# Kernel tuning notes

Hardware: AMD Instinct MI355X
Metric: run time of the kernel (lower is better)

## Reference

```python
import jax, jax.numpy as jnp
import numpy as np

B, S, D, NH, NKV, HD, FF = 2, 2048, 2048, 16, 8, 128, 8192
EPS = 1e-6
ROPE_THETA = 10000.0


def rmsnorm(x, w):
    return x * jax.lax.rsqrt(jnp.mean(x * x, axis=-1, keepdims=True) + EPS) * w


def rotate_half(x):
    h = x.shape[-1] // 2
    return jnp.concatenate([-x[..., h:], x[..., :h]], axis=-1)


def setup_inputs() -> dict:
    key = jax.random.key(0)
    ks = jax.random.split(key, 32)
    sc = 0.02
    inp = {}
    inp['x'] = jax.random.normal(ks[0], (B, S, D), dtype=jnp.float32)
    pos = jnp.arange(S, dtype=jnp.float32)
    inv = 1.0 / (ROPE_THETA ** (jnp.arange(0, HD, 2, dtype=jnp.float32) / HD))
    fr = jnp.outer(pos, inv)
    emb = jnp.concatenate([fr, fr], axis=-1)  # [S, HD]
    inp['cos'] = jnp.broadcast_to(jnp.cos(emb)[None], (B, S, HD)).astype(jnp.float32)
    inp['sin'] = jnp.broadcast_to(jnp.sin(emb)[None], (B, S, HD)).astype(jnp.float32)
    inp['vision_token_mask'] = jax.random.randint(ks[1], (B, S), 0, 2) > 0
    inp['attn_norm_w'] = jnp.ones((D,), jnp.float32)
    inp['ffn_norm_w'] = jnp.ones((D,), jnp.float32)
    shapes = {
        'wq': (D, NH * HD), 'wk': (D, NKV * HD), 'wv': (D, NKV * HD), 'wo': (NH * HD, D),
        'mm_wq': (D, NH * HD), 'mm_wk': (D, NKV * HD), 'mm_wv': (D, NKV * HD), 'mm_wo': (NH * HD, D),
        'gate_w': (D, FF), 'up_w': (D, FF), 'down_w': (FF, D),
        'mm_gate_w': (D, FF), 'mm_up_w': (D, FF), 'mm_down_w': (FF, D),
    }
    for i, (name, shp) in enumerate(shapes.items()):
        inp[name] = jax.random.normal(ks[2 + i], shp, dtype=jnp.float32) * sc
    for name in ['q_norm_w', 'k_norm_w', 'mm_q_norm_w', 'mm_k_norm_w']:
        inp[name] = jnp.ones((HD,), jnp.float32)
    return inp


def gpt_block(x, cos, sin, mask, attn_norm_w, ffn_norm_w,
              wq, wk, wv, wo, mm_wq, mm_wk, mm_wv, mm_wo,
              q_norm_w, k_norm_w, mm_q_norm_w, mm_k_norm_w,
              gate_w, up_w, down_w, mm_gate_w, mm_up_w, mm_down_w):
    m2 = mask[..., None]            # [B,S,1]
    m4 = mask[:, :, None, None]     # [B,S,1,1]
    h = rmsnorm(x, attn_norm_w)
    # dual-path QKV: text tokens use plain weights, vision tokens use mm_* weights
    q_t = rmsnorm((h @ wq).reshape(B, S, NH, HD), q_norm_w)
    q_v = rmsnorm((h @ mm_wq).reshape(B, S, NH, HD), mm_q_norm_w)
    q = jnp.where(m4, q_v, q_t)
    k_t = rmsnorm((h @ wk).reshape(B, S, NKV, HD), k_norm_w)
    k_v = rmsnorm((h @ mm_wk).reshape(B, S, NKV, HD), mm_k_norm_w)
    k = jnp.where(m4, k_v, k_t)
    v = jnp.where(m2, h @ mm_wv, h @ wv).reshape(B, S, NKV, HD)
    # RoPE (unsqueeze over head dim)
    cu = cos[:, :, None, :]
    su = sin[:, :, None, :]
    q = q * cu + rotate_half(q) * su
    k = k * cu + rotate_half(k) * su
    # GQA repeat + causal attention
    rep = NH // NKV
    k_r = jnp.repeat(k, rep, axis=2)
    v_r = jnp.repeat(v, rep, axis=2)
    scale = 1.0 / jnp.sqrt(jnp.float32(HD))
    scores = jnp.einsum('bqhd,bkhd->bhqk', q, k_r) * scale
    causal = jnp.tril(jnp.ones((S, S), bool))
    scores = jnp.where(causal, scores, jnp.float32(-1e30))
    p = jax.nn.softmax(scores, axis=-1)
    attn = jnp.einsum('bhqk,bkhd->bqhd', p, v_r).reshape(B, S, NH * HD)
    attn_out = jnp.where(m2, attn @ mm_wo, attn @ wo)
    h2 = x + attn_out
    # dual-path SwiGLU FFN
    g = rmsnorm(h2, ffn_norm_w)
    ff_t = (jax.nn.silu(g @ gate_w) * (g @ up_w)) @ down_w
    ff_v = (jax.nn.silu(g @ mm_gate_w) * (g @ mm_up_w)) @ mm_down_w
    return h2 + jnp.where(m2, ff_v, ff_t)


def reference(x, cos, sin, vision_token_mask, attn_norm_w, ffn_norm_w,
              wq, wk, wv, wo, mm_wq, mm_wk, mm_wv, mm_wo,
              q_norm_w, k_norm_w, mm_q_norm_w, mm_k_norm_w,
              gate_w, up_w, down_w, mm_gate_w, mm_up_w, mm_down_w):
    return gpt_block(x, cos, sin, vision_token_mask, attn_norm_w, ffn_norm_w,
                     wq, wk, wv, wo, mm_wq, mm_wk, mm_wv, mm_wo,
                     q_norm_w, k_norm_w, mm_q_norm_w, mm_k_norm_w,
                     gate_w, up_w, down_w, mm_gate_w, mm_up_w, mm_down_w)
```

## Files before the change

kernel.cpp:

```cpp
#include <hip/hip_runtime.h>

typedef unsigned short u16;
typedef __bf16 bf16x8 __attribute__((ext_vector_type(8)));
typedef float f32x4 __attribute__((ext_vector_type(4)));

__device__ __forceinline__ u16 f2bf(float f) {
    unsigned u = __builtin_bit_cast(unsigned, f);
    u += 0x7fffu + ((u >> 16) & 1u);
    return (u16)(u >> 16);
}
__device__ __forceinline__ float bf2f(u16 v) {
    unsigned u = ((unsigned)v) << 16;
    return __builtin_bit_cast(float, u);
}
__device__ __forceinline__ void glds16(const void* g, void* l) {
    __builtin_amdgcn_global_load_lds(
        (const __attribute__((address_space(1))) unsigned*)g,
        (__attribute__((address_space(3))) unsigned*)l, 16, 0, 0);
}

__global__ __launch_bounds__(1024) void build_perm(
    const int* __restrict__ mask, int* __restrict__ perm, int* __restrict__ counts)
{
    __shared__ int sc[1024];
    int t = threadIdx.x;
    int m[4], cnt = 0;
#pragma unroll
    for (int j = 0; j < 4; j++) {
        m[j] = mask[t * 4 + j] != 0;
        cnt += (m[j] == 0);
    }
    sc[t] = cnt;
    __syncthreads();
    for (int off = 1; off < 1024; off <<= 1) {
        int v = (t >= off) ? sc[t - off] : 0;
        __syncthreads();
        sc[t] += v;
        __syncthreads();
    }
    int totT = sc[1023];
    int exT = sc[t] - cnt;
    int exV = t * 4 - exT;
    int pT = exT, pV = totT + exV;
#pragma unroll
    for (int j = 0; j < 4; j++) {
        if (m[j] == 0) perm[pT++] = t * 4 + j;
        else           perm[pV++] = t * 4 + j;
    }
    if (t == 0) { counts[0] = totT; counts[1] = 4096 - totT; }
}

__global__ __launch_bounds__(256) void transpose_bf16(
    const float* __restrict__ W, u16* __restrict__ Wt, int Kd, int Nd)
{
    __shared__ float tile[32][33];
    int k0 = blockIdx.x * 32, n0 = blockIdx.y * 32;
    int tx = threadIdx.x, ty = threadIdx.y;
#pragma unroll
    for (int i = 0; i < 32; i += 8)
        tile[ty + i][tx] = W[(long)(k0 + ty + i) * Nd + n0 + tx];
    __syncthreads();
#pragma unroll
    for (int i = 0; i < 32; i += 8)
        Wt[(long)(n0 + ty + i) * Kd + k0 + tx] = f2bf(tile[tx][ty + i]);
}

__global__ __launch_bounds__(256) void rms_x(
    const float* __restrict__ x, const float* __restrict__ w, u16* __restrict__ out)
{
    long row = blockIdx.x;
    int t = threadIdx.x, wave = t >> 6, lane = t & 63;
    const float4* x4 = (const float4*)(x + row * 2048);
    float4 a = x4[2 * t], b = x4[2 * t + 1];
    float ss = a.x*a.x + a.y*a.y + a.z*a.z + a.w*a.w
             + b.x*b.x + b.y*b.y + b.z*b.z + b.w*b.w;
#pragma unroll
    for (int m = 1; m < 64; m <<= 1) ss += __shfl_xor(ss, m);
    __shared__ float red[4];
    if (lane == 0) red[wave] = ss;
    __syncthreads();
    float tot = red[0] + red[1] + red[2] + red[3];
    float inv = rsqrtf(tot * (1.0f / 2048.0f) + 1e-6f);
    const float4* w4 = (const float4*)w;
    float4 wa = w4[2 * t], wb = w4[2 * t + 1];
    u16* op = out + row * 2048 + t * 8;
    op[0] = f2bf(a.x * inv * wa.x); op[1] = f2bf(a.y * inv * wa.y);
    op[2] = f2bf(a.z * inv * wa.z); op[3] = f2bf(a.w * inv * wa.w);
    op[4] = f2bf(b.x * inv * wb.x); op[5] = f2bf(b.y * inv * wb.y);
    op[6] = f2bf(b.z * inv * wb.z); op[7] = f2bf(b.w * inv * wb.w);
}

template <int EPI, bool PG, bool PC>
__global__ __launch_bounds__(512, 2) void gemmk(
    const u16* __restrict__ A, const u16* __restrict__ Bt0, const u16* __restrict__ Bt1,
    void* __restrict__ Cv, const float* __restrict__ resid,
    const int* __restrict__ perm, const int* __restrict__ counts, int N, int K)
{
    extern __shared__ u16 lds[];
    const int nTn = N >> 8;
    const int nloc = nTn >> 3;
    const int xcd = blockIdx.x & 7, l = blockIdx.x >> 3;
    const int tn = xcd * nloc + (l % nloc);
    const int tm = l / nloc;
    const int nT = counts[0];
    const int tT = (nT + 127) >> 7, tV = (4096 - nT + 127) >> 7;
    if (tm >= tT + tV) return;
    const bool vis = tm >= tT;
    const u16* Bt = vis ? Bt1 : Bt0;
    const int rowbase = vis ? nT + (tm - tT) * 128 : tm * 128;
    const int rowlim = vis ? 4096 : nT;
    const int tid = threadIdx.x;
    const int wave = tid >> 6, lane = tid & 63;
    const int wrbase = (wave >> 2) * 64, wcbase = (wave & 3) * 64;
    const int lr = lane & 15, lg = lane >> 4;
    const int n0 = tn * 256;
    const int t8 = tid >> 3, sp = tid & 7;
    const char* aSrc[2];
    const char* bSrc[4];
#pragma unroll
    for (int c = 0; c < 2; c++) {
        int r = c * 64 + t8;
        int gr = rowbase + r; gr = gr < 4095 ? gr : 4095;
        long ar = PG ? perm[gr] : gr;
        aSrc[c] = (const char*)A + ar * (long)K * 2 + ((sp ^ (r & 7)) << 4);
    }
#pragma unroll
    for (int c = 0; c < 4; c++) {
        int r = c * 64 + t8;
        bSrc[c] = (const char*)Bt + (long)(n0 + r) * K * 2 + ((sp ^ (r & 7)) << 4);
    }
    auto stage = [&](int kt, int bu) {
        char* ab = (char*)lds + bu * 49152;
        char* bb = ab + 16384;
        long ko = (long)kt * 128;
#pragma unroll
        for (int c = 0; c < 2; c++)
            glds16(aSrc[c] + ko, ab + c * 8192 + tid * 16);
#pragma unroll
        for (int c = 0; c < 4; c++)
            glds16(bSrc[c] + ko, bb + c * 8192 + tid * 16);
    };
    auto ldA = [&](int bu, int mi, int kk) -> bf16x8 {
        const char* ab = (const char*)lds + bu * 49152;
        int row = wrbase + mi * 16 + lr;
        int sl = kk * 4 + lg;
        return *(const bf16x8*)(ab + row * 128 + ((sl ^ (row & 7)) << 4));
    };
    auto ldB = [&](int bu, int ni, int kk) -> bf16x8 {
        const char* bb = (const char*)lds + bu * 49152 + 16384;
        int row = wcbase + ni * 16 + lr;
        int sl = kk * 4 + lg;
        return *(const bf16x8*)(bb + row * 128 + ((sl ^ (row & 7)) << 4));
    };

    f32x4 acc[4][4] = {};
    const int nkt = K >> 6;
    stage(0, 0);
    stage(1, 1);
    for (int kt = 0; kt < nkt; ++kt) {
        const int bu = kt % 3;
        if (kt == nkt - 1) asm volatile("s_waitcnt vmcnt(0)" ::: "memory");
        else               asm volatile("s_waitcnt vmcnt(6)" ::: "memory");
        __builtin_amdgcn_s_barrier();
        if (kt + 2 < nkt) stage(kt + 2, (kt + 2) % 3);
#pragma unroll
        for (int kk = 0; kk < 2; kk++) {
            bf16x8 af[4], bq[4];
#pragma unroll
            for (int i = 0; i < 4; i++) af[i] = ldA(bu, i, kk);
#pragma unroll
            for (int j = 0; j < 4; j++) bq[j] = ldB(bu, j, kk);
            __builtin_amdgcn_s_setprio(1);
#pragma unroll
            for (int i = 0; i < 4; i++)
#pragma unroll
                for (int j = 0; j < 4; j++)
                    acc[i][j] = __builtin_amdgcn_mfma_f32_16x16x32_bf16(
                        af[i], bq[j], acc[i][j], 0, 0, 0);
            __builtin_amdgcn_s_setprio(0);
        }
    }
#pragma unroll
    for (int mi = 0; mi < 4; mi++)
#pragma unroll
        for (int r = 0; r < 4; r++) {
            int gr = rowbase + wrbase + mi * 16 + lg * 4 + r;
            if (gr >= rowlim) continue;
            long crow = PC ? (long)perm[gr] : (long)gr;
#pragma unroll
            for (int ni = 0; ni < 4; ni++) {
                long col = n0 + wcbase + ni * 16 + lr;
                long idx = crow * (long)N + col;
                float v = acc[mi][ni][r];
                if (EPI == 1)      ((u16*)Cv)[idx] = f2bf(v);
                else if (EPI == 2) ((float*)Cv)[idx] = resid[idx] + v;
                else if (EPI == 3) {
                    float g = bf2f(((u16*)Cv)[idx]);
                    ((u16*)Cv)[idx] = f2bf(g / (1.0f + __expf(-g)) * v);
                }
            }
        }
}

__global__ __launch_bounds__(256) void qk_fuse(
    const u16* __restrict__ p, const int* __restrict__ mask,
    const float* __restrict__ cs, const float* __restrict__ sn,
    const float* __restrict__ nwt, const float* __restrict__ nwv,
    u16* __restrict__ out, int H, int stride)
{
    int wave = threadIdx.x >> 6, lane = threadIdx.x & 63;
    int gw = blockIdx.x * 4 + wave;
    int tok = gw / H, h = gw % H;
    int b = tok >> 11, s = tok & 2047;
    const u16* src = p + (long)tok * stride + h * 128;
    const float* w = mask[tok] ? nwv : nwt;
    int d = lane * 2;
    float yx = bf2f(src[d]), yy = bf2f(src[d + 1]);
    float ss = yx * yx + yy * yy;
#pragma unroll
    for (int m = 1; m < 64; m <<= 1) ss += __shfl_xor(ss, m);
    float inv = rsqrtf(ss * (1.0f / 128.0f) + 1e-6f);
    float y0 = yx * inv * w[d], y1 = yy * inv * w[d + 1];
    float o0 = __shfl_xor(y0, 32), o1 = __shfl_xor(y1, 32);
    float sgn = (lane < 32) ? -1.0f : 1.0f;
    const float* cp = cs + (long)tok * 128 + d;
    const float* sp = sn + (long)tok * 128 + d;
    float r0 = y0 * cp[0] + sgn * o0 * sp[0];
    float r1 = y1 * cp[1] + sgn * o1 * sp[1];
    u16* op = out + (((long)b * H + h) * 2048 + s) * 128 + d;
    op[0] = f2bf(r0); op[1] = f2bf(r1);
}

__global__ __launch_bounds__(256) void v_fuse(
    const u16* __restrict__ vsrc, u16* __restrict__ outv)
{
    __shared__ u16 tile[32][33];
    int s0 = blockIdx.x * 32, d0 = blockIdx.y * 32;
    int bkv = blockIdx.z, b = bkv >> 3, kv = bkv & 7;
    int tx = threadIdx.x, ty = threadIdx.y;
#pragma unroll
    for (int i = 0; i < 32; i += 8) {
        long tok = (long)b * 2048 + s0 + ty + i;
        tile[ty + i][tx] = vsrc[tok * 2048 + kv * 128 + d0 + tx];
    }
    __syncthreads();
#pragma unroll
    for (int i = 0; i < 32; i += 8)
        outv[(((long)b * 8 + kv) * 128 + d0 + ty + i) * 2048 + s0 + tx] =
            tile[tx][ty + i];
}

__global__ __launch_bounds__(256) void attn_fwd(
    const u16* __restrict__ q, const u16* __restrict__ k,
    const u16* __restrict__ v, u16* __restrict__ out)
{
    __shared__ u16 Ks[32 * 128];
    __shared__ u16 Vs[128 * 32];
    __shared__ u16 Ps[4][16][40];
    const int tid = threadIdx.x, wave = tid >> 6, lane = tid & 63;
    const int lr = lane & 15, lg = lane >> 4;
    const int b = blockIdx.z, h = blockIdx.y, q0 = blockIdx.x * 64;
    const int kvh = h >> 1;
    const u16* qp = q + (((long)b * 16 + h) * 2048 + q0 + wave * 16) * 128;
    bf16x8 qf[4];
#pragma unroll
    for (int f = 0; f < 4; f++)
        qf[f] = *(const bf16x8*)(qp + (long)lr * 128 + f * 32 + lg * 8);
    const char* kbase = (const char*)(k + ((long)b * 8 + kvh) * 2048 * 128);
    const char* vbase = (const char*)(v + ((long)b * 8 + kvh) * 128 * 2048);
    f32x4 o[8] = {};
    float lsum[4] = {};
    const float sc2 = 0.08838834764831845f * 1.44269504088896f;
    const float MB = 16.5f;
    const int ntiles = (q0 + 64) >> 5;
    for (int t = 0; t < ntiles; ++t) {
        int kv0 = t * 32;
        __syncthreads();
#pragma unroll
        for (int j = 0; j < 2; j++) {
            int L = (j * 4 + wave) * 1024 + lane * 16;
            {
                int row = L >> 8, cb = L & 255;
                glds16(kbase + (long)(kv0 + row) * 256 + (cb ^ ((row & 7) << 4)),
                       (char*)Ks + (j * 4 + wave) * 1024);
            }
            {
                int row = L >> 6, cb = L & 63;
                glds16(vbase + (long)row * 4096 + kv0 * 2 + (cb ^ ((row & 3) << 4)),
                       (char*)Vs + (j * 4 + wave) * 1024);
            }
        }
        __syncthreads();
        f32x4 s[2] = {};
#pragma unroll
        for (int sub = 0; sub < 2; ++sub)
#pragma unroll
            for (int f = 0; f < 4; ++f) {
                int row = sub * 16 + lr;
                int cb = (f * 64 + lg * 16) ^ ((row & 7) << 4);
                bf16x8 kf = *(const bf16x8*)((const char*)Ks + row * 256 + cb);
                s[sub] = __builtin_amdgcn_mfma_f32_16x16x32_bf16(qf[f], kf, s[sub], 0, 0, 0);
            }
#pragma unroll
        for (int r = 0; r < 4; r++) {
            int rowg = q0 + wave * 16 + lg * 4 + r;
            float s0 = s[0][r] * sc2 - MB; if (kv0 + lr > rowg)      s0 = -1e30f;
            float s1 = s[1][r] * sc2 - MB; if (kv0 + 16 + lr > rowg) s1 = -1e30f;
            float p0 = exp2f(s0), p1 = exp2f(s1);
            lsum[r] += p0 + p1;
            int prow = lg * 4 + r;
            Ps[wave][prow][lr] = f2bf(p0);
            Ps[wave][prow][16 + lr] = f2bf(p1);
        }
        bf16x8 pf = *(const bf16x8*)&Ps[wave][lr][lg * 8];
#pragma unroll
        for (int ni = 0; ni < 8; ni++) {
            int row = ni * 16 + lr;
            int cb = (lg * 16) ^ ((row & 3) << 4);
            bf16x8 vf = *(const bf16x8*)((const char*)Vs + row * 64 + cb);
            o[ni] = __builtin_amdgcn_mfma_f32_16x16x32_bf16(pf, vf, o[ni], 0, 0, 0);
        }
    }
#pragma unroll
    for (int r = 0; r < 4; r++)
#pragma unroll
        for (int mm = 1; mm < 16; mm <<= 1) lsum[r] += __shfl_xor(lsum[r], mm);
#pragma unroll
    for (int ni = 0; ni < 8; ni++)
#pragma unroll
        for (int r = 0; r < 4; r++) {
            long row = (long)b * 2048 + q0 + wave * 16 + lg * 4 + r;
            out[row * 2048 + h * 128 + ni * 16 + lr] = f2bf(o[ni][r] / lsum[r]);
        }
}

extern "C" void kernel_launch(void* const* d_in, const int* in_sizes, int n_in,
                              void* d_out, int out_size, void* d_ws, size_t ws_size,
                              hipStream_t stream)
{
    const float* x    = (const float*)d_in[0];
    const float* cosp = (const float*)d_in[1];
    const float* sinp = (const float*)d_in[2];
    const int*   mask = (const int*)d_in[3];
    const float* anw  = (const float*)d_in[4];
    const float* fnw  = (const float*)d_in[5];
    const float* wq   = (const float*)d_in[6];
    const float* wk   = (const float*)d_in[7];
    const float* wv   = (const float*)d_in[8];
    const float* wo   = (const float*)d_in[9];
    const float* mwq  = (const float*)d_in[10];
    const float* mwk  = (const float*)d_in[11];
    const float* mwv  = (const float*)d_in[12];
    const float* mwo  = (const float*)d_in[13];
    const float* gw   = (const float*)d_in[14];
    const float* uw   = (const float*)d_in[15];
    const float* dw   = (const float*)d_in[16];
    const float* mgw  = (const float*)d_in[17];
    const float* muw  = (const float*)d_in[18];
    const float* mdw  = (const float*)d_in[19];
    const float* qnw  = (const float*)d_in[20];
    const float* knw  = (const float*)d_in[21];
    const float* mqnw = (const float*)d_in[22];
    const float* mknw = (const float*)d_in[23];

    char* base = (char*)d_ws;
    u16* wT0   = (u16*)(base);
    u16* wT1   = (u16*)(base + (32u << 20));
    u16* hbf   = (u16*)(base + (64u << 20));
    u16* qb    = (u16*)(base + (64u << 20));
    u16* qq    = (u16*)(base + (80u << 20));
    u16* kvb   = (u16*)(base + (96u << 20));
    u16* kb    = (u16*)(base + (112u << 20));
    u16* vb    = (u16*)(base + (120u << 20));
    u16* attnb = (u16*)(base + (128u << 20));
    u16* e1    = (u16*)(base + (80u << 20));
    float* h2  = (float*)(base + (144u << 20));
    u16* gbf   = (u16*)(base + (176u << 20));
    int* perm  = (int*)(base + (192u << 20));
    int* cnts  = perm + 4096;

    hipFuncSetAttribute((const void*)&gemmk<1, true, true>,
                        hipFuncAttributeMaxDynamicSharedMemorySize, 147456);
    hipFuncSetAttribute((const void*)&gemmk<2, true, true>,
                        hipFuncAttributeMaxDynamicSharedMemorySize, 147456);
    hipFuncSetAttribute((const void*)&gemmk<1, true, false>,
                        hipFuncAttributeMaxDynamicSharedMemorySize, 147456);
    hipFuncSetAttribute((const void*)&gemmk<3, true, false>,
                        hipFuncAttributeMaxDynamicSharedMemorySize, 147456);
    hipFuncSetAttribute((const void*)&gemmk<2, false, true>,
                        hipFuncAttributeMaxDynamicSharedMemorySize, 147456);

    dim3 tb(32, 8);
    auto TR = [&](const float* w, u16* dst, int K, int N) {
        transpose_bf16<<<dim3(K / 32, N / 32), tb, 0, stream>>>(w, dst, K, N);
    };

    build_perm<<<1, 1024, 0, stream>>>(mask, perm, cnts);
    rms_x<<<4096, 256, 0, stream>>>(x, anw, hbf);

    TR(wq, wT0, 2048, 2048); TR(mwq, wT1, 2048, 2048);
    gemmk<1, true, true><<<264, 512, 147456, stream>>>(
        hbf, wT0, wT1, (void*)qq, nullptr, perm, cnts, 2048, 2048);
    TR(wk, wT0, 2048, 1024); TR(wv, wT0 + 1024 * 2048, 2048, 1024);
    TR(mwk, wT1, 2048, 1024); TR(mwv, wT1 + 1024 * 2048, 2048, 1024);
    gemmk<1, true, true><<<264, 512, 147456, stream>>>(
        hbf, wT0, wT1, (void*)kvb, nullptr, perm, cnts, 2048, 2048);

    qk_fuse<<<16384, 256, 0, stream>>>(qq, mask, cosp, sinp, qnw, mqnw, qb, 16, 2048);
    qk_fuse<<<8192, 256, 0, stream>>>(kvb, mask, cosp, sinp, knw, mknw, kb, 8, 2048);
    v_fuse<<<dim3(64, 4, 16), tb, 0, stream>>>(kvb + 1024, vb);

    attn_fwd<<<dim3(32, 16, 2), 256, 0, stream>>>(qb, kb, vb, attnb);

    TR(wo, wT0, 2048, 2048); TR(mwo, wT1, 2048, 2048);
    gemmk<2, true, true><<<264, 512, 147456, stream>>>(
        attnb, wT0, wT1, (void*)h2, x, perm, cnts, 2048, 2048);

    rms_x<<<4096, 256, 0, stream>>>(h2, fnw, gbf);

    TR(gw, wT0, 2048, 8192); TR(mgw, wT1, 2048, 8192);
    gemmk<1, true, false><<<1056, 512, 147456, stream>>>(
        gbf, wT0, wT1, (void*)e1, nullptr, perm, cnts, 8192, 2048);
    TR(uw, wT0, 2048, 8192); TR(muw, wT1, 2048, 8192);
    gemmk<3, true, false><<<1056, 512, 147456, stream>>>(
        gbf, wT0, wT1, (void*)e1, nullptr, perm, cnts, 8192, 2048);
    TR(dw, wT0, 8192, 2048); TR(mdw, wT1, 8192, 2048);
    gemmk<2, false, true><<<264, 512, 147456, stream>>>(
        e1, wT0, wT1, (void*)d_out, h2, perm, cnts, 2048, 8192);
}
```

Baseline: 1.225 ms.

## Fuse gate/up GEMMs with SwiGLU epilogue, merge QKV GEMM, remap XCD tiles

Merges the Q and KV projections into one GEMM over a concatenated 4096-wide weight, so the normalized activations are read once and there is one launch fewer. Replaces the separate gate GEMM and the up GEMM with a read-modify-write epilogue by a single gemm_gu kernel. It computes both accumulators on a 128-wide N tile and applies SiLU*up in registers, which removes the bf16 round trip of the gate output. Adds an xcd_map that groups M tiles in chunks of eight per XCD for better L2 reuse. The workspace layout is enlarged to hold two weight buffers at once, and the hardcoded TM=33 assumes 4096 tokens.

```diff
diff --git a/kernel.cpp b/kernel.cpp
--- a/kernel.cpp
+++ b/kernel.cpp
@@ -17,6 +17,21 @@
     __builtin_amdgcn_global_load_lds(
         (const __attribute__((address_space(1))) unsigned*)g,
         (__attribute__((address_space(3))) unsigned*)l, 16, 0, 0);
+}
+
+__device__ __forceinline__ void xcd_map(int bid, int nloc, int& tm, int& tn)
+{
+    const int TM = 33;
+    const int xcd = bid & 7;
+    int l = bid >> 3;
+    const int per = nloc << 3;
+    const int fullC = TM >> 3;
+    const int lFull = fullC * per;
+    int c, tn_l, tmIn;
+    if (l < lFull) { c = l / per; int r = l - c * per; tn_l = r >> 3; tmIn = r & 7; }
+    else { int r = l - lFull; int sc = TM - (fullC << 3); c = fullC; tn_l = r / sc; tmIn = r % sc; }
+    tm = (c << 3) + tmIn;
+    tn = xcd * nloc + tn_l;
 }
 
 __global__ __launch_bounds__(1024) void build_perm(
@@ -97,11 +112,8 @@
     const int* __restrict__ perm, const int* __restrict__ counts, int N, int K)
 {
     extern __shared__ u16 lds[];
-    const int nTn = N >> 8;
-    const int nloc = nTn >> 3;
-    const int xcd = blockIdx.x & 7, l = blockIdx.x >> 3;
-    const int tn = xcd * nloc + (l % nloc);
-    const int tm = l / nloc;
+    int tm, tn;
+    xcd_map(blockIdx.x, N >> 11, tm, tn);
     const int nT = counts[0];
     const int tT = (nT + 127) >> 7, tV = (4096 - nT + 127) >> 7;
     if (tm >= tT + tV) return;
@@ -194,10 +206,104 @@
                 float v = acc[mi][ni][r];
                 if (EPI == 1)      ((u16*)Cv)[idx] = f2bf(v);
                 else if (EPI == 2) ((float*)Cv)[idx] = resid[idx] + v;
-                else if (EPI == 3) {
-                    float g = bf2f(((u16*)Cv)[idx]);
-                    ((u16*)Cv)[idx] = f2bf(g / (1.0f + __expf(-g)) * v);
+            }
+        }
+}
+
+__global__ __launch_bounds__(512, 2) void gemm_gu(
+    const u16* __restrict__ A,
+    const u16* __restrict__ Bg0, const u16* __restrict__ Bg1,
+    const u16* __restrict__ Bu0, const u16* __restrict__ Bu1,
+    u16* __restrict__ C,
+    const int* __restrict__ perm, const int* __restrict__ counts, int N, int K)
+{
+    extern __shared__ u16 lds[];
+    int tm, tn;
+    xcd_map(blockIdx.x, N >> 10, tm, tn);
+    const int nT = counts[0];
+    const int tT = (nT + 127) >> 7, tV = (4096 - nT + 127) >> 7;
+    if (tm >= tT + tV) return;
+    const bool vis = tm >= tT;
+    const u16* Bg = vis ? Bg1 : Bg0;
+    const u16* Bu = vis ? Bu1 : Bu0;
+    const int rowbase = vis ? nT + (tm - tT) * 128 : tm * 128;
+    const int rowlim = vis ? 4096 : nT;
+    const int tid = threadIdx.x;
+    const int wave = tid >> 6, lane = tid & 63;
+    const int wrbase = (wave >> 2) * 64, wcbase = (wave & 3) * 32;
+    const int lr = lane & 15, lg = lane >> 4;
+    const int n0 = tn * 128;
+    const int t8 = tid >> 3, sp = tid & 7;
+    const char *aSrc[2], *gSrc[2], *uSrc[2];
+#pragma unroll
+    for (int c = 0; c < 2; c++) {
+        int r = c * 64 + t8;
+        int gr = rowbase + r; gr = gr < 4095 ? gr : 4095;
+        long ar = (long)perm[gr];
+        aSrc[c] = (const char*)A + ar * (long)K * 2 + ((sp ^ (r & 7)) << 4);
+        gSrc[c] = (const char*)Bg + (long)(n0 + r) * K * 2 + ((sp ^ (r & 7)) << 4);
+        uSrc[c] = (const char*)Bu + (long)(n0 + r) * K * 2 + ((sp ^ (r & 7)) << 4);
+    }
+    auto stage = [&](int kt, int bu) {
+        char* ab = (char*)lds + bu * 49152;
+        long ko = (long)kt * 128;
+#pragma unroll
+        for (int c = 0; c < 2; c++) {
+            glds16(aSrc[c] + ko, ab + c * 8192 + tid * 16);
+            glds16(gSrc[c] + ko, ab + 16384 + c * 8192 + tid * 16);
+            glds16(uSrc[c] + ko, ab + 32768 + c * 8192 + tid * 16);
+        }
+    };
+    auto ld = [&](int bu, int sub, int row, int kk) -> bf16x8 {
+        const char* p = (const char*)lds + bu * 49152 + sub * 16384;
+        int sl = kk * 4 + lg;
+        return *(const bf16x8*)(p + row * 128 + ((sl ^ (row & 7)) << 4));
+    };
+
+    f32x4 accg[4][2] = {}, accu[4][2] = {};
+    const int nkt = K >> 6;
+    stage(0, 0);
+    stage(1, 1);
+    for (int kt = 0; kt < nkt; ++kt) {
+        const int bu = kt % 3;
+        if (kt == nkt - 1) asm volatile("s_waitcnt vmcnt(0)" ::: "memory");
+        else               asm volatile("s_waitcnt vmcnt(6)" ::: "memory");
+        __builtin_amdgcn_s_barrier();
+        if (kt + 2 < nkt) stage(kt + 2, (kt + 2) % 3);
+#pragma unroll
+        for (int kk = 0; kk < 2; kk++) {
+            bf16x8 af[4], bg[2], bv[2];
+#pragma unroll
+            for (int i = 0; i < 4; i++) af[i] = ld(bu, 0, wrbase + i * 16 + lr, kk);
+#pragma unroll
+            for (int j = 0; j < 2; j++) {
+                bg[j] = ld(bu, 1, wcbase + j * 16 + lr, kk);
+                bv[j] = ld(bu, 2, wcbase + j * 16 + lr, kk);
+            }
+            __builtin_amdgcn_s_setprio(1);
+#pragma unroll
+            for (int i = 0; i < 4; i++)
+#pragma unroll
+                for (int j = 0; j < 2; j++) {
+                    accg[i][j] = __builtin_amdgcn_mfma_f32_16x16x32_bf16(
+                        af[i], bg[j], accg[i][j], 0, 0, 0);
+                    accu[i][j] = __builtin_amdgcn_mfma_f32_16x16x32_bf16(
+                        af[i], bv[j], accu[i][j], 0, 0, 0);
                 }
+            __builtin_amdgcn_s_setprio(0);
+        }
+    }
+#pragma unroll
+    for (int mi = 0; mi < 4; mi++)
+#pragma unroll
+        for (int r = 0; r < 4; r++) {
+            int gr = rowbase + wrbase + mi * 16 + lg * 4 + r;
+            if (gr >= rowlim) continue;
+#pragma unroll
+            for (int ni = 0; ni < 2; ni++) {
+                long col = n0 + wcbase + ni * 16 + lr;
+                float g = accg[mi][ni][r], u = accu[mi][ni][r];
+                C[(long)gr * N + col] = f2bf(g / (1.0f + __expf(-g)) * u);
             }
         }
 }
@@ -232,7 +338,7 @@
 }
 
 __global__ __launch_bounds__(256) void v_fuse(
-    const u16* __restrict__ vsrc, u16* __restrict__ outv)
+    const u16* __restrict__ vsrc, u16* __restrict__ outv, int stride)
 {
     __shared__ u16 tile[32][33];
     int s0 = blockIdx.x * 32, d0 = blockIdx.y * 32;
@@ -241,7 +347,7 @@
 #pragma unroll
     for (int i = 0; i < 32; i += 8) {
         long tok = (long)b * 2048 + s0 + ty + i;
-        tile[ty + i][tx] = vsrc[tok * 2048 + kv * 128 + d0 + tx];
+        tile[ty + i][tx] = vsrc[tok * stride + kv * 128 + d0 + tx];
     }
     __syncthreads();
 #pragma unroll
@@ -364,30 +470,29 @@
     const float* mknw = (const float*)d_in[23];
 
     char* base = (char*)d_ws;
-    u16* wT0   = (u16*)(base);
-    u16* wT1   = (u16*)(base + (32u << 20));
+    u16* wA0   = (u16*)(base);
+    u16* wA1   = (u16*)(base + (32u << 20));
+    u16* wB0   = (u16*)(base + (64u << 20));
+    u16* wB1   = (u16*)(base + (96u << 20));
     u16* hbf   = (u16*)(base + (64u << 20));
-    u16* qb    = (u16*)(base + (64u << 20));
-    u16* qq    = (u16*)(base + (80u << 20));
-    u16* kvb   = (u16*)(base + (96u << 20));
-    u16* kb    = (u16*)(base + (112u << 20));
-    u16* vb    = (u16*)(base + (120u << 20));
-    u16* attnb = (u16*)(base + (128u << 20));
-    u16* e1    = (u16*)(base + (80u << 20));
-    float* h2  = (float*)(base + (144u << 20));
-    u16* gbf   = (u16*)(base + (176u << 20));
-    int* perm  = (int*)(base + (192u << 20));
+    u16* qkv   = (u16*)(base + (80u << 20));
+    u16* qb    = (u16*)(base + (112u << 20));
+    u16* kb    = (u16*)(base + (128u << 20));
+    u16* vb    = (u16*)(base + (136u << 20));
+    u16* attnb = (u16*)(base + (144u << 20));
+    u16* e1    = (u16*)(base + (128u << 20));
+    float* h2  = (float*)(base + (192u << 20));
+    u16* gbf   = (u16*)(base + (224u << 20));
+    int* perm  = (int*)(base + (240u << 20));
     int* cnts  = perm + 4096;
 
     hipFuncSetAttribute((const void*)&gemmk<1, true, true>,
                         hipFuncAttributeMaxDynamicSharedMemorySize, 147456);
     hipFuncSetAttribute((const void*)&gemmk<2, true, true>,
                         hipFuncAttributeMaxDynamicSharedMemorySize, 147456);
-    hipFuncSetAttribute((const void*)&gemmk<1, true, false>,
+    hipFuncSetAttribute((const void*)&gemmk<2, false, true>,
                         hipFuncAttributeMaxDynamicSharedMemorySize, 147456);
-    hipFuncSetAttribute((const void*)&gemmk<3, true, false>,
-                        hipFuncAttributeMaxDynamicSharedMemorySize, 147456);
-    hipFuncSetAttribute((const void*)&gemmk<2, false, true>,
+    hipFuncSetAttribute((const void*)&gemm_gu,
                         hipFuncAttributeMaxDynamicSharedMemorySize, 147456);
 
     dim3 tb(32, 8);
@@ -398,33 +503,32 @@
     build_perm<<<1, 1024, 0, stream>>>(mask, perm, cnts);
     rms_x<<<4096, 256, 0, stream>>>(x, anw, hbf);
 
-    TR(wq, wT0, 2048, 2048); TR(mwq, wT1, 2048, 2048);
-    gemmk<1, true, true><<<264, 512, 147456, stream>>>(
-        hbf, wT0, wT1, (void*)qq, nullptr, perm, cnts, 2048, 2048);
-    TR(wk, wT0, 2048, 1024); TR(wv, wT0 + 1024 * 2048, 2048, 1024);
-    TR(mwk, wT1, 2048, 1024); TR(mwv, wT1 + 1024 * 2048, 2048, 1024);
-    gemmk<1, true, true><<<264, 512, 147456, stream>>>(
-        hbf, wT0, wT1, (void*)kvb, nullptr, perm, cnts, 2048, 2048);
-
-    qk_fuse<<<16384, 256, 0, stream>>>(qq, mask, cosp, sinp, qnw, mqnw, qb, 16, 2048);
-    qk_fuse<<<8192, 256, 0, stream>>>(kvb, mask, cosp, sinp, knw, mknw, kb, 8, 2048);
-    v_fuse<<<dim3(64, 4, 16), tb, 0, stream>>>(kvb + 1024, vb);
+    TR(wq, wA0, 2048, 2048);
+    TR(wk, wA0 + (long)2048 * 2048, 2048, 1024);
+    TR(wv, wA0 + (long)3072 * 2048, 2048, 1024);
+    TR(mwq, wA1, 2048, 2048);
+    TR(mwk, wA1 + (long)2048 * 2048, 2048, 1024);
+    TR(mwv, wA1 + (long)3072 * 2048, 2048, 1024);
+    gemmk<1, true, true><<<528, 512, 147456, stream>>>(
+        hbf, wA0, wA1, (void*)qkv, nullptr, perm, cnts, 4096, 2048);
+
+    qk_fuse<<<16384, 256, 0, stream>>>(qkv, mask, cosp, sinp, qnw, mqnw, qb, 16, 4096);
+    qk_fuse<<<8192, 256, 0, stream>>>(qkv + 2048, mask, cosp, sinp, knw, mknw, kb, 8, 4096);
+    v_fuse<<<dim3(64, 4, 16), tb, 0, stream>>>(qkv + 3072, vb, 4096);
 
     attn_fwd<<<dim3(32, 16, 2), 256, 0, stream>>>(qb, kb, vb, attnb);
 
-    TR(wo, wT0, 2048, 2048); TR(mwo, wT1, 2048, 2048);
+    TR(wo, wA0, 2048, 2048); TR(mwo, wA1, 2048, 2048);
     gemmk<2, true, true><<<264, 512, 147456, stream>>>(
-        attnb, wT0, wT1, (void*)h2, x, perm, cnts, 2048, 2048);
+        attnb, wA0, wA1, (void*)h2, x, perm, cnts, 2048, 2048);
 
     rms_x<<<4096, 256, 0, stream>>>(h2, fnw, gbf);
 
-    TR(gw, wT0, 2048, 8192); TR(mgw, wT1, 2048, 8192);
-    gemmk<1, true, false><<<1056, 512, 147456, stream>>>(
-        gbf, wT0, wT1, (void*)e1, nullptr, perm, cnts, 8192, 2048);
-    TR(uw, wT0, 2048, 8192); TR(muw, wT1, 2048, 8192);
-    gemmk<3, true, false><<<1056, 512, 147456, stream>>>(
-        gbf, wT0, wT1, (void*)e1, nullptr, perm, cnts, 8192, 2048);
-    TR(dw, wT0, 8192, 2048); TR(mdw, wT1, 8192, 2048);
+    TR(gw, wA0, 2048, 8192); TR(mgw, wA1, 2048, 8192);
+    TR(uw, wB0, 2048, 8192); TR(muw, wB1, 2048, 8192);
+    gemm_gu<<<2112, 512, 147456, stream>>>(
+        gbf, wA0, wA1, wB0, wB1, e1, perm, cnts, 8192, 2048);
+    TR(dw, wA0, 8192, 2048); TR(mdw, wA1, 8192, 2048);
     gemmk<2, false, true><<<264, 512, 147456, stream>>>(
-        e1, wT0, wT1, (void*)d_out, h2, perm, cnts, 2048, 8192);
-}
+        e1, wA0, wA1, (void*)d_out, h2, perm, cnts, 2048, 8192);
+}
```

Result: faster. 1.155 ms (-5.7%).
